# Kernel tuning notes

Measured on AMD Instinct MI355X. Metric: run time of the kernel, lower is better.

Reference implementation:

```python
import jax, jax.numpy as jnp
import numpy as np

HEADS = 4
DIM_HEAD = 32
SCALE = DIM_HEAD ** -0.5
EPS = 1e-5


def setup_inputs() -> dict:
    key = jax.random.key(0)
    ks = jax.random.split(key, 4)
    x = jax.random.normal(ks[0], (8, 64, 32, 32, 32), dtype=jnp.float32)
    w_qkv = jax.random.normal(ks[1], (384, 64), dtype=jnp.float32) * 0.05
    w_out = jax.random.normal(ks[2], (64, 128), dtype=jnp.float32) * 0.05
    b_out = jax.random.normal(ks[3], (64,), dtype=jnp.float32) * 0.05
    gamma = jnp.ones((64,), dtype=jnp.float32)
    beta = jnp.zeros((64,), dtype=jnp.float32)
    return {"x": x, "w_qkv": w_qkv, "w_out": w_out, "b_out": b_out,
            "gamma": gamma, "beta": beta}


def reference(x, w_qkv, w_out, b_out, gamma, beta):
    b, c, l, h, w = x.shape
    n = l * h * w
    xf = x.reshape(b, c, n)
    # 1x1 Conv3d (no bias) == channel matmul
    qkv = jnp.einsum('oc,bcn->bon', w_qkv, xf)            # [b, 3*H*D, n]
    q, k, v = jnp.split(qkv, 3, axis=1)
    def to_heads(t):
        return t.reshape(b, HEADS, DIM_HEAD, n)            # [b, H, D, n]
    q, k, v = to_heads(q), to_heads(k), to_heads(v)
    q = jax.nn.softmax(q, axis=2) * SCALE                  # softmax over head dim
    k = jax.nn.softmax(k, axis=3)                          # softmax over tokens
    context = jnp.einsum('bhdn,bhen->bhde', k, v)          # [b, H, D, D]
    out = jnp.einsum('bhde,bhdn->bhen', context, q)        # [b, H, D, n]
    out = out.reshape(b, HEADS * DIM_HEAD, n)
    # to_out: 1x1 Conv3d with bias, then GroupNorm(1, dim)
    out = jnp.einsum('oc,bcn->bon', w_out, out) + b_out[None, :, None]
    mu = out.mean(axis=(1, 2), keepdims=True)
    var = out.var(axis=(1, 2), keepdims=True)
    out = (out - mu) * jax.lax.rsqrt(var + EPS)
    out = out * gamma[None, :, None] + beta[None, :, None]
    return out.reshape(b, c, l, h, w)
```

## Files before the change

### kernel.cpp

```cpp
#include <hip/hip_runtime.h>

typedef __bf16 bf16;
typedef __bf16 bf16x4 __attribute__((ext_vector_type(4)));
typedef __bf16 bf16x8 __attribute__((ext_vector_type(8)));
typedef float f32x4 __attribute__((ext_vector_type(4)));

#define NTOK 32768
#define SCALE_F 0.17677669529663689f

__global__ __launch_bounds__(256) void k1_ctx(const float* __restrict__ x,
    const float* __restrict__ wqkv, float* __restrict__ ctx, float* __restrict__ s1)
{
  const int b = blockIdx.y, chunk = blockIdx.x;
  const int t = threadIdx.x, w = t>>6, l = t&63, lr = l&15, lg = l>>4;
  __shared__ bf16 xT[64*72];
  __shared__ bf16 ek[128*72];
  __shared__ bf16 vl[128*72];

  bf16x8 bw[4][2];
  #pragma unroll
  for (int ct=0;ct<4;ct++)
    #pragma unroll
    for (int ks=0;ks<2;ks++){
      const float* src = wqkv + (128 + w*64 + ct*16 + lr)*64 + ks*32 + lg*8;
      #pragma unroll
      for (int j=0;j<8;j++) bw[ct][ks][j] = (bf16)src[j];
    }
  bf16x8 ones;
  #pragma unroll
  for (int j=0;j<8;j++) ones[j] = (bf16)1.0f;

  f32x4 ctxa[2][2]; f32x4 s1a[2];
  #pragma unroll
  for (int i=0;i<2;i++){
    s1a[i] = f32x4{0.f,0.f,0.f,0.f};
    #pragma unroll
    for (int j=0;j<2;j++) ctxa[i][j] = f32x4{0.f,0.f,0.f,0.f};
  }
  const float* xb = x + (long)b*64*NTOK;
  bf16* dst = (w<2) ? ek : vl;
  const int chb = (w&1)*64;
  const bool isk = (w<2);
  const int sn = t&63, cg16 = (t>>6)*16;

  bf16x8 t0, t1;
  {
    const int n0 = chunk*512;
    #pragma unroll
    for (int i=0;i<8;i++) t0[i] = (bf16)xb[(long)(cg16+i)*NTOK + n0 + sn];
    #pragma unroll
    for (int i=0;i<8;i++) t1[i] = (bf16)xb[(long)(cg16+8+i)*NTOK + n0 + sn];
  }

  for (int s=0; s<8; s++) {
    *(bf16x8*)&xT[sn*72 + cg16]     = t0;
    *(bf16x8*)&xT[sn*72 + cg16 + 8] = t1;
    __syncthreads();
    if (s+1 < 8){
      const int n0 = chunk*512 + (s+1)*64;
      #pragma unroll
      for (int i=0;i<8;i++) t0[i] = (bf16)xb[(long)(cg16+i)*NTOK + n0 + sn];
      #pragma unroll
      for (int i=0;i<8;i++) t1[i] = (bf16)xb[(long)(cg16+8+i)*NTOK + n0 + sn];
    }
    f32x4 acc[4][4];
    #pragma unroll
    for (int rt=0;rt<4;rt++)
      #pragma unroll
      for (int ct=0;ct<4;ct++) acc[rt][ct] = f32x4{0.f,0.f,0.f,0.f};
    #pragma unroll
    for (int ks=0;ks<2;ks++){
      bf16x8 af[4];
      #pragma unroll
      for (int rt=0;rt<4;rt++)
        af[rt] = *(const bf16x8*)&xT[(rt*16+lr)*72 + ks*32 + lg*8];
      #pragma unroll
      for (int rt=0;rt<4;rt++)
        #pragma unroll
        for (int ct=0;ct<4;ct++)
          acc[rt][ct] = __builtin_amdgcn_mfma_f32_16x16x32_bf16(af[rt], bw[ct][ks], acc[rt][ct], 0,0,0);
    }
    #pragma unroll
    for (int ct=0;ct<4;ct++){
      const int row = chb + ct*16 + lr;
      #pragma unroll
      for (int rt=0;rt<4;rt++){
        bf16x4 p;
        #pragma unroll
        for (int ri=0;ri<4;ri++){
          const float v = acc[rt][ct][ri];
          p[ri] = isk ? (bf16)__expf(v) : (bf16)v;
        }
        *(bf16x4*)&dst[row*72 + rt*16 + lg*4] = p;
      }
    }
    __syncthreads();
    #pragma unroll
    for (int ks=0;ks<2;ks++){
      bf16x8 bd[2];
      #pragma unroll
      for (int cd=0;cd<2;cd++)
        bd[cd] = *(const bf16x8*)&ek[(w*32 + cd*16 + lr)*72 + ks*32 + lg*8];
      #pragma unroll
      for (int re=0;re<2;re++){
        bf16x8 a = *(const bf16x8*)&vl[(w*32 + re*16 + lr)*72 + ks*32 + lg*8];
        #pragma unroll
        for (int cd=0;cd<2;cd++)
          ctxa[re][cd] = __builtin_amdgcn_mfma_f32_16x16x32_bf16(a, bd[cd], ctxa[re][cd], 0,0,0);
      }
      #pragma unroll
      for (int cd=0;cd<2;cd++)
        s1a[cd] = __builtin_amdgcn_mfma_f32_16x16x32_bf16(ones, bd[cd], s1a[cd], 0,0,0);
    }
  }
  float* cp = ctx + ((long)b*4 + w)*1024;
  #pragma unroll
  for (int re=0;re<2;re++)
    #pragma unroll
    for (int cd=0;cd<2;cd++)
      #pragma unroll
      for (int ri=0;ri<4;ri++){
        const int e = re*16 + lg*4 + ri, d = cd*16 + lr;
        atomicAdd(&cp[e*32 + d], ctxa[re][cd][ri]);
      }
  if (lg==0){
    #pragma unroll
    for (int cd=0;cd<2;cd++)
      atomicAdd(&s1[(long)b*128 + w*32 + cd*16 + lr], s1a[cd][0]);
  }
}

__global__ __launch_bounds__(256) void k2_w2(const float* __restrict__ ctx,
    const float* __restrict__ s1, const float* __restrict__ wout, bf16* __restrict__ W2)
{
  const int b = blockIdx.y, h = blockIdx.x, t = threadIdx.x;
  __shared__ float cs[1024];
  __shared__ float s1s[32];
  {
    f32x4 p4 = *(const f32x4*)(ctx + ((long)b*4 + h)*1024 + t*4);
    *(f32x4*)&cs[t*4] = p4;
  }
  if (t < 32) s1s[t] = s1[(long)b*128 + h*32 + t];
  __syncthreads();
  const int d = t & 31;
  const float rinv = SCALE_F / s1s[d];
  #pragma unroll
  for (int oi=0; oi<8; oi++){
    const int o = (t>>5)*8 + oi;
    float acc = 0.f;
    #pragma unroll
    for (int e=0;e<32;e++) acc += wout[o*128 + h*32 + e] * cs[e*32 + d];
    W2[((long)b*64 + o)*128 + h*32 + d] = (bf16)(acc * rinv);
  }
}

__global__ __launch_bounds__(256,2) void k3_y(const float* __restrict__ x,
    const float* __restrict__ wqkv, const bf16* __restrict__ W2g,
    const float* __restrict__ bout, bf16* __restrict__ ybf, float* __restrict__ yacc)
{
  const int b = blockIdx.y, blk = blockIdx.x;
  const int t = threadIdx.x, w = t>>6, l = t&63, lr = l&15, lg = l>>4;
  __shared__ bf16 W2s[64*136];
  __shared__ bf16 xT[64*72];
  __shared__ bf16 qs[64*136];
  __shared__ float red[8];
  const float* xb = x + (long)b*64*NTOK;
  bf16* yb = ybf + (long)b*64*NTOK;

  bf16x8 qfr[2][2];
  #pragma unroll
  for (int rt=0;rt<2;rt++)
    #pragma unroll
    for (int ks=0;ks<2;ks++){
      const float* src = wqkv + (w*32 + rt*16 + lr)*64 + ks*32 + lg*8;
      #pragma unroll
      for (int j=0;j<8;j++) qfr[rt][ks][j] = (bf16)src[j];
    }
  {
    const bf16* src = W2g + (long)b*8192 + t*32;
    const int o = t>>2, c0 = (t&3)*32;
    #pragma unroll
    for (int k=0;k<4;k++)
      *(bf16x8*)&W2s[o*136 + c0 + k*8] = *(const bf16x8*)(src + k*8);
  }
  float boutr[16];
  #pragma unroll
  for (int rt=0;rt<4;rt++)
    #pragma unroll
    for (int ri=0;ri<4;ri++) boutr[rt*4+ri] = bout[rt*16 + lg*4 + ri];

  const int sn = t&63, cg16 = (t>>6)*16;
  bf16x8 t0, t1;
  {
    const int n0 = blk*512;
    #pragma unroll
    for (int i=0;i<8;i++) t0[i] = (bf16)xb[(long)(cg16+i)*NTOK + n0 + sn];
    #pragma unroll
    for (int i=0;i<8;i++) t1[i] = (bf16)xb[(long)(cg16+8+i)*NTOK + n0 + sn];
  }
  float sum=0.f, ss=0.f;

  for (int ti=0; ti<8; ti++){
    const int n0 = blk*512 + ti*64;
    *(bf16x8*)&xT[sn*72 + cg16]     = t0;
    *(bf16x8*)&xT[sn*72 + cg16 + 8] = t1;
    __syncthreads();
    if (ti+1 < 8){
      const int nn0 = n0 + 64;
      #pragma unroll
      for (int i=0;i<8;i++) t0[i] = (bf16)xb[(long)(cg16+i)*NTOK + nn0 + sn];
      #pragma unroll
      for (int i=0;i<8;i++) t1[i] = (bf16)xb[(long)(cg16+8+i)*NTOK + nn0 + sn];
    }
    f32x4 qa[2][4];
    #pragma unroll
    for (int rt=0;rt<2;rt++)
      #pragma unroll
      for (int ct=0;ct<4;ct++) qa[rt][ct] = f32x4{0.f,0.f,0.f,0.f};
    #pragma unroll
    for (int ks=0;ks<2;ks++){
      bf16x8 bfr[4];
      #pragma unroll
      for (int ct=0;ct<4;ct++)
        bfr[ct] = *(const bf16x8*)&xT[(ct*16+lr)*72 + ks*32 + lg*8];
      #pragma unroll
      for (int rt=0;rt<2;rt++)
        #pragma unroll
        for (int ct=0;ct<4;ct++)
          qa[rt][ct] = __builtin_amdgcn_mfma_f32_16x16x32_bf16(qfr[rt][ks], bfr[ct], qa[rt][ct], 0,0,0);
    }
    #pragma unroll
    for (int ct=0;ct<4;ct++){
      float e[2][4]; float p = 0.f;
      #pragma unroll
      for (int rt=0;rt<2;rt++)
        #pragma unroll
        for (int ri=0;ri<4;ri++){ e[rt][ri] = __expf(qa[rt][ct][ri]); p += e[rt][ri]; }
      p += __shfl_xor(p, 16, 64);
      p += __shfl_xor(p, 32, 64);
      const float rinv = 1.f/p;
      const int nn = ct*16 + lr;
      #pragma unroll
      for (int rt=0;rt<2;rt++){
        bf16x4 pk;
        #pragma unroll
        for (int ri=0;ri<4;ri++) pk[ri] = (bf16)(e[rt][ri]*rinv);
        *(bf16x4*)&qs[nn*136 + w*32 + rt*16 + lg*4] = pk;
      }
    }
    __syncthreads();
    f32x4 ya[4];
    #pragma unroll
    for (int rt=0;rt<4;rt++) ya[rt] = f32x4{0.f,0.f,0.f,0.f};
    #pragma unroll
    for (int ks=0;ks<4;ks++){
      bf16x8 bq = *(const bf16x8*)&qs[(w*16+lr)*136 + ks*32 + lg*8];
      #pragma unroll
      for (int rt=0;rt<4;rt++){
        bf16x8 a = *(const bf16x8*)&W2s[(rt*16+lr)*136 + ks*32 + lg*8];
        ya[rt] = __builtin_amdgcn_mfma_f32_16x16x32_bf16(a, bq, ya[rt], 0,0,0);
      }
    }
    #pragma unroll
    for (int rt=0;rt<4;rt++)
      #pragma unroll
      for (int ri=0;ri<4;ri++){
        const int o = rt*16 + lg*4 + ri;
        const float val = ya[rt][ri] + boutr[rt*4+ri];
        sum += val; ss += val*val;
        yb[(long)o*NTOK + n0 + w*16 + lr] = (bf16)val;
      }
    __syncthreads();
  }
  #pragma unroll
  for (int off=1; off<64; off<<=1){
    sum += __shfl_xor(sum, off, 64);
    ss  += __shfl_xor(ss,  off, 64);
  }
  if (l==0){ red[w*2] = sum; red[w*2+1] = ss; }
  __syncthreads();
  if (t==0){
    atomicAdd(&yacc[b*2],   red[0]+red[2]+red[4]+red[6]);
    atomicAdd(&yacc[b*2+1], red[1]+red[3]+red[5]+red[7]);
  }
}

__global__ __launch_bounds__(256) void k4_norm(const bf16* __restrict__ ybf,
    const float* __restrict__ yacc, const float* __restrict__ gamma,
    const float* __restrict__ beta, float* __restrict__ out)
{
  const long idx = ((long)blockIdx.x*256 + threadIdx.x)*8;
  const int b = (int)(idx >> 21);
  const int c = (int)((idx >> 15) & 63);
  const float inv_n = 1.f/2097152.f;
  const float mu  = yacc[b*2]*inv_n;
  const float inv = rsqrtf(yacc[b*2+1]*inv_n - mu*mu + 1e-5f);
  const float g = gamma[c]*inv;
  const float be = beta[c] - mu*g;
  bf16x8 v8 = *(const bf16x8*)(ybf + idx);
  f32x4 o0, o1;
  #pragma unroll
  for (int j=0;j<4;j++){ o0[j] = (float)v8[j]*g + be; o1[j] = (float)v8[4+j]*g + be; }
  *(f32x4*)(out + idx)     = o0;
  *(f32x4*)(out + idx + 4) = o1;
}

extern "C" void kernel_launch(void* const* d_in, const int* in_sizes, int n_in,
                              void* d_out, int out_size, void* d_ws, size_t ws_size,
                              hipStream_t stream) {
  const float* x     = (const float*)d_in[0];
  const float* wqkv  = (const float*)d_in[1];
  const float* wout  = (const float*)d_in[2];
  const float* bout  = (const float*)d_in[3];
  const float* gamma = (const float*)d_in[4];
  const float* beta  = (const float*)d_in[5];
  float* out = (float*)d_out;
  char* ws = (char*)d_ws;
  if (ws_size < 33820736u) return;

  float* ctx  = (float*)(ws + 0);
  float* s1   = (float*)(ws + 131072);
  float* yacc = (float*)(ws + 135168);
  bf16*  W2   = (bf16*) (ws + 135232);
  bf16*  ybf  = (bf16*) (ws + 266304);

  hipMemsetAsync(ws, 0, 135232, stream);
  k1_ctx <<<dim3(64,8), 256, 0, stream>>>(x, wqkv, ctx, s1);
  k2_w2  <<<dim3(4,8),  256, 0, stream>>>(ctx, s1, wout, W2);
  k3_y   <<<dim3(64,8), 256, 0, stream>>>(x, wqkv, W2, bout, ybf, yacc);
  k4_norm<<<8192,       256, 0, stream>>>(ybf, yacc, gamma, beta, out);
}
```

Measured before the change: 100.8 us.

## Compute softmaxed Q in the context kernel and recompute output GEMM for stats

```diff
diff --git a/kernel.cpp b/kernel.cpp
--- a/kernel.cpp
+++ b/kernel.cpp
@@ -8,8 +8,9 @@
 #define NTOK 32768
 #define SCALE_F 0.17677669529663689f
 
-__global__ __launch_bounds__(256) void k1_ctx(const float* __restrict__ x,
-    const float* __restrict__ wqkv, float* __restrict__ ctx, float* __restrict__ s1)
+__global__ __launch_bounds__(256) void k1_all(const float* __restrict__ x,
+    const float* __restrict__ wqkv, float* __restrict__ ctx, float* __restrict__ s1,
+    bf16* __restrict__ qsg)
 {
   const int b = blockIdx.y, chunk = blockIdx.x;
   const int t = threadIdx.x, w = t>>6, l = t&63, lr = l&15, lg = l>>4;
@@ -26,6 +27,15 @@
       #pragma unroll
       for (int j=0;j<8;j++) bw[ct][ks][j] = (bf16)src[j];
     }
+  bf16x8 qfr[2][2];
+  #pragma unroll
+  for (int rt=0;rt<2;rt++)
+    #pragma unroll
+    for (int ks=0;ks<2;ks++){
+      const float* src = wqkv + (w*32 + rt*16 + lr)*64 + ks*32 + lg*8;
+      #pragma unroll
+      for (int j=0;j<8;j++) qfr[rt][ks][j] = (bf16)src[j];
+    }
   bf16x8 ones;
   #pragma unroll
   for (int j=0;j<8;j++) ones[j] = (bf16)1.0f;
@@ -53,21 +63,27 @@
   }
 
   for (int s=0; s<8; s++) {
+    const int n0 = chunk*512 + s*64;
     *(bf16x8*)&xT[sn*72 + cg16]     = t0;
     *(bf16x8*)&xT[sn*72 + cg16 + 8] = t1;
     __syncthreads();
     if (s+1 < 8){
-      const int n0 = chunk*512 + (s+1)*64;
-      #pragma unroll
-      for (int i=0;i<8;i++) t0[i] = (bf16)xb[(long)(cg16+i)*NTOK + n0 + sn];
-      #pragma unroll
-      for (int i=0;i<8;i++) t1[i] = (bf16)xb[(long)(cg16+8+i)*NTOK + n0 + sn];
+      const int nn0 = n0 + 64;
+      #pragma unroll
+      for (int i=0;i<8;i++) t0[i] = (bf16)xb[(long)(cg16+i)*NTOK + nn0 + sn];
+      #pragma unroll
+      for (int i=0;i<8;i++) t1[i] = (bf16)xb[(long)(cg16+8+i)*NTOK + nn0 + sn];
     }
     f32x4 acc[4][4];
+    f32x4 qa[2][4];
     #pragma unroll
     for (int rt=0;rt<4;rt++)
       #pragma unroll
       for (int ct=0;ct<4;ct++) acc[rt][ct] = f32x4{0.f,0.f,0.f,0.f};
+    #pragma unroll
+    for (int rt=0;rt<2;rt++)
+      #pragma unroll
+      for (int ct=0;ct<4;ct++) qa[rt][ct] = f32x4{0.f,0.f,0.f,0.f};
     #pragma unroll
     for (int ks=0;ks<2;ks++){
       bf16x8 af[4];
@@ -79,6 +95,13 @@
         #pragma unroll
         for (int ct=0;ct<4;ct++)
           acc[rt][ct] = __builtin_amdgcn_mfma_f32_16x16x32_bf16(af[rt], bw[ct][ks], acc[rt][ct], 0,0,0);
+      if (qsg){
+        #pragma unroll
+        for (int rt=0;rt<2;rt++)
+          #pragma unroll
+          for (int ct=0;ct<4;ct++)
+            qa[rt][ct] = __builtin_amdgcn_mfma_f32_16x16x32_bf16(qfr[rt][ks], af[ct], qa[rt][ct], 0,0,0);
+      }
     }
     #pragma unroll
     for (int ct=0;ct<4;ct++){
@@ -95,6 +118,27 @@
       }
     }
     __syncthreads();
+    if (qsg){
+      #pragma unroll
+      for (int ct=0;ct<4;ct++){
+        float e[2][4]; float p = 0.f;
+        #pragma unroll
+        for (int rt=0;rt<2;rt++)
+          #pragma unroll
+          for (int ri=0;ri<4;ri++){ e[rt][ri] = __expf(qa[rt][ct][ri]); p += e[rt][ri]; }
+        p += __shfl_xor(p, 16, 64);
+        p += __shfl_xor(p, 32, 64);
+        const float rinv = 1.f/p;
+        const long nrow = (long)b*NTOK + n0 + ct*16 + lr;
+        #pragma unroll
+        for (int rt=0;rt<2;rt++){
+          bf16x4 pk;
+          #pragma unroll
+          for (int ri=0;ri<4;ri++) pk[ri] = (bf16)(e[rt][ri]*rinv);
+          *(bf16x4*)(qsg + nrow*128 + w*32 + rt*16 + lg*4) = pk;
+        }
+      }
+    }
     #pragma unroll
     for (int ks=0;ks<2;ks++){
       bf16x8 bd[2];
@@ -151,6 +195,112 @@
     #pragma unroll
     for (int e=0;e<32;e++) acc += wout[o*128 + h*32 + e] * cs[e*32 + d];
     W2[((long)b*64 + o)*128 + h*32 + d] = (bf16)(acc * rinv);
+  }
+}
+
+__global__ __launch_bounds__(256) void k3_stats(const bf16* __restrict__ qsg,
+    const bf16* __restrict__ W2g, const float* __restrict__ bout,
+    float* __restrict__ yacc)
+{
+  const int b = blockIdx.y, blk = blockIdx.x;
+  const int t = threadIdx.x, w = t>>6, l = t&63, lr = l&15, lg = l>>4;
+  const bf16* Wb = W2g + (long)b*8192;
+  bf16x8 wa[4][4];
+  #pragma unroll
+  for (int rt=0;rt<4;rt++)
+    #pragma unroll
+    for (int ks=0;ks<4;ks++)
+      wa[rt][ks] = *(const bf16x8*)(Wb + (rt*16+lr)*128 + ks*32 + lg*8);
+  float boutr[16];
+  #pragma unroll
+  for (int rt=0;rt<4;rt++)
+    #pragma unroll
+    for (int ri=0;ri<4;ri++) boutr[rt*4+ri] = bout[rt*16 + lg*4 + ri];
+  const bf16* qb = qsg + ((long)b*NTOK + blk*256 + w*64)*128;
+  float sum=0.f, ss=0.f;
+  #pragma unroll
+  for (int ct=0;ct<4;ct++){
+    const bf16* qrow = qb + (ct*16+lr)*128 + lg*8;
+    bf16x8 bq[4];
+    #pragma unroll
+    for (int ks=0;ks<4;ks++) bq[ks] = *(const bf16x8*)(qrow + ks*32);
+    f32x4 a4[4];
+    #pragma unroll
+    for (int rt=0;rt<4;rt++) a4[rt] = f32x4{0.f,0.f,0.f,0.f};
+    #pragma unroll
+    for (int ks=0;ks<4;ks++)
+      #pragma unroll
+      for (int rt=0;rt<4;rt++)
+        a4[rt] = __builtin_amdgcn_mfma_f32_16x16x32_bf16(wa[rt][ks], bq[ks], a4[rt], 0,0,0);
+    #pragma unroll
+    for (int rt=0;rt<4;rt++)
+      #pragma unroll
+      for (int ri=0;ri<4;ri++){
+        const float v = a4[rt][ri] + boutr[rt*4+ri];
+        sum += v; ss += v*v;
+      }
+  }
+  #pragma unroll
+  for (int off=1; off<64; off<<=1){
+    sum += __shfl_xor(sum, off, 64);
+    ss  += __shfl_xor(ss,  off, 64);
+  }
+  if (l==0){
+    atomicAdd(&yacc[b*2],   sum);
+    atomicAdd(&yacc[b*2+1], ss);
+  }
+}
+
+__global__ __launch_bounds__(256) void k4_gemm(const bf16* __restrict__ qsg,
+    const bf16* __restrict__ W2g, const float* __restrict__ bout,
+    const float* __restrict__ yacc, const float* __restrict__ gamma,
+    const float* __restrict__ beta, float* __restrict__ out)
+{
+  const int b = blockIdx.y, blk = blockIdx.x;
+  const int t = threadIdx.x, w = t>>6, l = t&63, lr = l&15, lg = l>>4;
+  const bf16* Wb = W2g + (long)b*8192;
+  bf16x8 wa[4][4];
+  #pragma unroll
+  for (int rt=0;rt<4;rt++)
+    #pragma unroll
+    for (int ks=0;ks<4;ks++)
+      wa[rt][ks] = *(const bf16x8*)(Wb + (rt*16+lr)*128 + ks*32 + lg*8);
+  const float inv_n = 1.f/2097152.f;
+  const float mu  = yacc[b*2]*inv_n;
+  const float inv = rsqrtf(yacc[b*2+1]*inv_n - mu*mu + 1e-5f);
+  float ga[16], be2[16];
+  #pragma unroll
+  for (int rt=0;rt<4;rt++)
+    #pragma unroll
+    for (int ri=0;ri<4;ri++){
+      const int o = rt*16 + lg*4 + ri;
+      const float g = gamma[o]*inv;
+      ga[rt*4+ri]  = g;
+      be2[rt*4+ri] = beta[o] - mu*g + bout[o]*g;
+    }
+  const int nb = blk*256 + w*64;
+  const bf16* qb = qsg + ((long)b*NTOK + nb)*128;
+  float* ob = out + (long)b*64*NTOK;
+  #pragma unroll
+  for (int ct=0;ct<4;ct++){
+    const bf16* qrow = qb + (ct*16+lr)*128 + lg*8;
+    bf16x8 bq[4];
+    #pragma unroll
+    for (int ks=0;ks<4;ks++) bq[ks] = *(const bf16x8*)(qrow + ks*32);
+    f32x4 a4[4];
+    #pragma unroll
+    for (int rt=0;rt<4;rt++) a4[rt] = f32x4{0.f,0.f,0.f,0.f};
+    #pragma unroll
+    for (int ks=0;ks<4;ks++)
+      #pragma unroll
+      for (int rt=0;rt<4;rt++)
+        a4[rt] = __builtin_amdgcn_mfma_f32_16x16x32_bf16(wa[rt][ks], bq[ks], a4[rt], 0,0,0);
+    #pragma unroll
+    for (int rt=0;rt<4;rt++)
+      #pragma unroll
+      for (int ri=0;ri<4;ri++)
+        ob[(long)(rt*16+lg*4+ri)*NTOK + nb + ct*16 + lr] =
+            a4[rt][ri]*ga[rt*4+ri] + be2[rt*4+ri];
   }
 }
 
@@ -322,11 +472,22 @@
   float* s1   = (float*)(ws + 131072);
   float* yacc = (float*)(ws + 135168);
   bf16*  W2   = (bf16*) (ws + 135232);
-  bf16*  ybf  = (bf16*) (ws + 266304);
-
+  char*  big0 = ws + 266304;
+
+  const bool big = (ws_size >= 67375168ull);
   hipMemsetAsync(ws, 0, 135232, stream);
-  k1_ctx <<<dim3(64,8), 256, 0, stream>>>(x, wqkv, ctx, s1);
-  k2_w2  <<<dim3(4,8),  256, 0, stream>>>(ctx, s1, wout, W2);
-  k3_y   <<<dim3(64,8), 256, 0, stream>>>(x, wqkv, W2, bout, ybf, yacc);
-  k4_norm<<<8192,       256, 0, stream>>>(ybf, yacc, gamma, beta, out);
-}
+
+  if (big){
+    bf16* qsg = (bf16*)big0;
+    k1_all  <<<dim3(64,8),  256, 0, stream>>>(x, wqkv, ctx, s1, qsg);
+    k2_w2   <<<dim3(4,8),   256, 0, stream>>>(ctx, s1, wout, W2);
+    k3_stats<<<dim3(128,8), 256, 0, stream>>>(qsg, W2, bout, yacc);
+    k4_gemm <<<dim3(128,8), 256, 0, stream>>>(qsg, W2, bout, yacc, gamma, beta, out);
+  } else {
+    bf16* ybf = (bf16*)big0;
+    k1_all  <<<dim3(64,8), 256, 0, stream>>>(x, wqkv, ctx, s1, (bf16*)nullptr);
+    k2_w2   <<<dim3(4,8),  256, 0, stream>>>(ctx, s1, wout, W2);
+    k3_y    <<<dim3(64,8), 256, 0, stream>>>(x, wqkv, W2, bout, ybf, yacc);
+    k4_norm <<<8192,       256, 0, stream>>>(ybf, yacc, gamma, beta, out);
+  }
+}
```

New measurement: 224.0 us. 2.22x slower.

## Double-buffer k3 shared tiles, keep W2 fragments in registers, drop trailing barrier

Applied to the files above, without the earlier changes.

```diff
diff --git a/kernel.cpp b/kernel.cpp
--- a/kernel.cpp
+++ b/kernel.cpp
@@ -154,15 +154,14 @@
   }
 }
 
-__global__ __launch_bounds__(256,2) void k3_y(const float* __restrict__ x,
+__global__ __launch_bounds__(256,1) void k3_y(const float* __restrict__ x,
     const float* __restrict__ wqkv, const bf16* __restrict__ W2g,
     const float* __restrict__ bout, bf16* __restrict__ ybf, float* __restrict__ yacc)
 {
   const int b = blockIdx.y, blk = blockIdx.x;
   const int t = threadIdx.x, w = t>>6, l = t&63, lr = l&15, lg = l>>4;
-  __shared__ bf16 W2s[64*136];
-  __shared__ bf16 xT[64*72];
-  __shared__ bf16 qs[64*136];
+  __shared__ bf16 xT[2][64*72];
+  __shared__ bf16 qs[2][64*136];
   __shared__ float red[8];
   const float* xb = x + (long)b*64*NTOK;
   bf16* yb = ybf + (long)b*64*NTOK;
@@ -176,13 +175,12 @@
       #pragma unroll
       for (int j=0;j<8;j++) qfr[rt][ks][j] = (bf16)src[j];
     }
-  {
-    const bf16* src = W2g + (long)b*8192 + t*32;
-    const int o = t>>2, c0 = (t&3)*32;
-    #pragma unroll
-    for (int k=0;k<4;k++)
-      *(bf16x8*)&W2s[o*136 + c0 + k*8] = *(const bf16x8*)(src + k*8);
-  }
+  bf16x8 wa[4][4];
+  #pragma unroll
+  for (int rt=0;rt<4;rt++)
+    #pragma unroll
+    for (int ks=0;ks<4;ks++)
+      wa[rt][ks] = *(const bf16x8*)(W2g + (long)b*8192 + (rt*16+lr)*128 + ks*32 + lg*8);
   float boutr[16];
   #pragma unroll
   for (int rt=0;rt<4;rt++)
@@ -200,10 +198,12 @@
   }
   float sum=0.f, ss=0.f;
 
+  #pragma unroll
   for (int ti=0; ti<8; ti++){
+    const int p = ti & 1;
     const int n0 = blk*512 + ti*64;
-    *(bf16x8*)&xT[sn*72 + cg16]     = t0;
-    *(bf16x8*)&xT[sn*72 + cg16 + 8] = t1;
+    *(bf16x8*)&xT[p][sn*72 + cg16]     = t0;
+    *(bf16x8*)&xT[p][sn*72 + cg16 + 8] = t1;
     __syncthreads();
     if (ti+1 < 8){
       const int nn0 = n0 + 64;
@@ -222,7 +222,7 @@
       bf16x8 bfr[4];
       #pragma unroll
       for (int ct=0;ct<4;ct++)
-        bfr[ct] = *(const bf16x8*)&xT[(ct*16+lr)*72 + ks*32 + lg*8];
+        bfr[ct] = *(const bf16x8*)&xT[p][(ct*16+lr)*72 + ks*32 + lg*8];
       #pragma unroll
       for (int rt=0;rt<2;rt++)
         #pragma unroll
@@ -231,21 +231,21 @@
     }
     #pragma unroll
     for (int ct=0;ct<4;ct++){
-      float e[2][4]; float p = 0.f;
+      float e[2][4]; float pp = 0.f;
       #pragma unroll
       for (int rt=0;rt<2;rt++)
         #pragma unroll
-        for (int ri=0;ri<4;ri++){ e[rt][ri] = __expf(qa[rt][ct][ri]); p += e[rt][ri]; }
-      p += __shfl_xor(p, 16, 64);
-      p += __shfl_xor(p, 32, 64);
-      const float rinv = 1.f/p;
+        for (int ri=0;ri<4;ri++){ e[rt][ri] = __expf(qa[rt][ct][ri]); pp += e[rt][ri]; }
+      pp += __shfl_xor(pp, 16, 64);
+      pp += __shfl_xor(pp, 32, 64);
+      const float rinv = 1.f/pp;
       const int nn = ct*16 + lr;
       #pragma unroll
       for (int rt=0;rt<2;rt++){
         bf16x4 pk;
         #pragma unroll
         for (int ri=0;ri<4;ri++) pk[ri] = (bf16)(e[rt][ri]*rinv);
-        *(bf16x4*)&qs[nn*136 + w*32 + rt*16 + lg*4] = pk;
+        *(bf16x4*)&qs[p][nn*136 + w*32 + rt*16 + lg*4] = pk;
       }
     }
     __syncthreads();
@@ -254,12 +254,10 @@
     for (int rt=0;rt<4;rt++) ya[rt] = f32x4{0.f,0.f,0.f,0.f};
     #pragma unroll
     for (int ks=0;ks<4;ks++){
-      bf16x8 bq = *(const bf16x8*)&qs[(w*16+lr)*136 + ks*32 + lg*8];
-      #pragma unroll
-      for (int rt=0;rt<4;rt++){
-        bf16x8 a = *(const bf16x8*)&W2s[(rt*16+lr)*136 + ks*32 + lg*8];
-        ya[rt] = __builtin_amdgcn_mfma_f32_16x16x32_bf16(a, bq, ya[rt], 0,0,0);
-      }
+      bf16x8 bq = *(const bf16x8*)&qs[p][(w*16+lr)*136 + ks*32 + lg*8];
+      #pragma unroll
+      for (int rt=0;rt<4;rt++)
+        ya[rt] = __builtin_amdgcn_mfma_f32_16x16x32_bf16(wa[rt][ks], bq, ya[rt], 0,0,0);
     }
     #pragma unroll
     for (int rt=0;rt<4;rt++)
@@ -270,7 +268,6 @@
         sum += val; ss += val*val;
         yb[(long)o*NTOK + n0 + w*16 + lr] = (bf16)val;
       }
-    __syncthreads();
   }
   #pragma unroll
   for (int off=1; off<64; off<<=1){
```

New measurement: 121.0 us. 1.2x slower.
